# Optimization experiments

Measured on AMD Instinct MI355X. Metric: run time of the kernel, lower is better.

Reference implementation:

```python
import jax, jax.numpy as jnp
import numpy as np

B, S, D, H, F = 2, 2048, 1024, 16, 4096
DK = D // H
EPS = 1e-6


def _ln(x, g, b):
    mu = jnp.mean(x, axis=-1, keepdims=True)
    var = jnp.mean(jnp.square(x - mu), axis=-1, keepdims=True)
    return (x - mu) * jax.lax.rsqrt(var + EPS) * g + b


def setup_inputs() -> dict:
    key = jax.random.key(0)
    ks = jax.random.split(key, 8)
    sc = 0.02
    return {
        "x": jax.random.normal(ks[0], (B, S, D), jnp.float32),
        "wq": jax.random.normal(ks[1], (D, D), jnp.float32) * sc,
        "bq": jnp.zeros((D,), jnp.float32),
        "wk": jax.random.normal(ks[2], (D, D), jnp.float32) * sc,
        "bk": jnp.zeros((D,), jnp.float32),
        "wv": jax.random.normal(ks[3], (D, D), jnp.float32) * sc,
        "bv": jnp.zeros((D,), jnp.float32),
        "wo": jax.random.normal(ks[4], (D, D), jnp.float32) * sc,
        "bo": jnp.zeros((D,), jnp.float32),
        "w1": jax.random.normal(ks[5], (D, F), jnp.float32) * sc,
        "b1": jnp.zeros((F,), jnp.float32),
        "w2": jax.random.normal(ks[6], (F, D), jnp.float32) * sc,
        "b2": jnp.zeros((D,), jnp.float32),
        "g1": jnp.ones((D,), jnp.float32),
        "be1": jnp.zeros((D,), jnp.float32),
        "g2": jnp.ones((D,), jnp.float32),
        "be2": jnp.zeros((D,), jnp.float32),
    }


def reference(x, wq, bq, wk, bk, wv, bv, wo, bo, w1, b1, w2, b2, g1, be1, g2, be2):
    # Multi-head self-attention (no masks, eval-mode dropout = identity)
    q = (x @ wq + bq).reshape(B, S, H, DK)
    k = (x @ wk + bk).reshape(B, S, H, DK)
    v = (x @ wv + bv).reshape(B, S, H, DK)
    scale = 1.0 / (DK ** 0.5)
    score = jnp.einsum('bihd,bjhd->bhij', q, k) * scale  # [B,H,S,S]
    p = jax.nn.softmax(score, axis=-1)
    attn = jnp.einsum('bhij,bjhd->bihd', p, v).reshape(B, S, D)
    attn = attn @ wo + bo
    # residual + LayerNorm 1
    h = _ln(x + attn, g1, be1)
    # FFN (relu) + residual + LayerNorm 2
    ff = jax.nn.relu(h @ w1 + b1) @ w2 + b2
    return _ln(h + ff, g2, be2)
```

## Files before the change

### kernel.cpp

```cpp
#include <hip/hip_runtime.h>
#include <hip/hip_bf16.h>
#include <cmath>

typedef __bf16 bf16_t;
typedef __bf16 bf16x4 __attribute__((ext_vector_type(4)));
typedef __bf16 bf16x8 __attribute__((ext_vector_type(8)));
typedef float  f32x4  __attribute__((ext_vector_type(4)));

__device__ __forceinline__ void gld_lds16(const bf16_t* g, bf16_t* l) {
    __builtin_amdgcn_global_load_lds(
        (const __attribute__((address_space(1))) void*)g,
        (__attribute__((address_space(3))) void*)l,
        16, 0, 0);
}

__global__ __launch_bounds__(256) void cast_bf16_k(const float* __restrict__ in,
                                                   bf16_t* __restrict__ out, int n4) {
    int i = blockIdx.x * 256 + threadIdx.x;
    if (i >= n4) return;
    f32x4 v = ((const f32x4*)in)[i];
    bf16x4 o;
    o[0] = (bf16_t)v[0]; o[1] = (bf16_t)v[1]; o[2] = (bf16_t)v[2]; o[3] = (bf16_t)v[3];
    ((bf16x4*)out)[i] = o;
}

__global__ __launch_bounds__(256) void transpose_cast(const float* __restrict__ in,
                                                      bf16_t* __restrict__ out,
                                                      int K, int N) {
    __shared__ float tile[32][33];
    int n0 = blockIdx.x * 32, k0 = blockIdx.y * 32;
    int tx = threadIdx.x & 31;
    int ty = threadIdx.x >> 5;
#pragma unroll
    for (int i = 0; i < 4; i++) {
        int kk = ty + i * 8;
        tile[kk][tx] = in[(size_t)(k0 + kk) * N + n0 + tx];
    }
    __syncthreads();
#pragma unroll
    for (int i = 0; i < 4; i++) {
        int nn = ty + i * 8;
        out[(size_t)(n0 + nn) * K + k0 + tx] = (bf16_t)tile[tx][nn];
    }
}

template<int MT>
__global__ __launch_bounds__(256) void gemm_bt(const bf16_t* __restrict__ A,
                                               const bf16_t* __restrict__ Bt,
                                               const float* __restrict__ bias,
                                               float* __restrict__ Cf,
                                               bf16_t* __restrict__ Cb,
                                               int M, int N, int K, int relu,
                                               int nbm, int nbn) {
    constexpr int TM = MT * 32;
    __shared__ __attribute__((aligned(16))) bf16_t As[TM * 32];
    __shared__ __attribute__((aligned(16))) bf16_t Bs[128 * 32];
    const int tid  = threadIdx.x;
    const int lane = tid & 63;
    const int wave = tid >> 6;
    const int wm = wave & 1, wn = wave >> 1;

    const int span  = 8 * nbn;
    const int group = blockIdx.x / span;
    const int rem   = blockIdx.x % span;
    const int bm    = group * 8 + (rem & 7);
    const int bn    = rem >> 3;

    const int r4 = tid >> 2;
    const int kc = (tid & 3) * 8;
    const bf16_t* Ag = A  + (size_t)(bm * TM  + r4) * K + kc;
    const bf16_t* Bg = Bt + (size_t)(bn * 128 + r4) * K + kc;
    bf16_t* Asl = As + tid * 8;
    bf16_t* Bsl = Bs + tid * 8;

    f32x4 acc[MT][4] = {};
    const int mrow = lane & 15;
    const int q8   = (lane >> 4) * 8;

    for (int k0 = 0; k0 < K; k0 += 32) {
        __syncthreads();
#pragma unroll
        for (int i = 0; i < MT / 2; i++)
            gld_lds16(Ag + (size_t)(i * 64) * K + k0, Asl + i * 64 * 32);
        gld_lds16(Bg + k0,                  Bsl);
        gld_lds16(Bg + (size_t)64 * K + k0, Bsl + 64 * 32);
        __syncthreads();

        bf16x8 af[MT], bfr[4];
#pragma unroll
        for (int mt = 0; mt < MT; mt++)
            af[mt] = *(const bf16x8*)(As + (wm * (MT * 16) + mt * 16 + mrow) * 32 + q8);
#pragma unroll
        for (int nt = 0; nt < 4; nt++)
            bfr[nt] = *(const bf16x8*)(Bs + (wn * 64 + nt * 16 + mrow) * 32 + q8);
#pragma unroll
        for (int mt = 0; mt < MT; mt++)
#pragma unroll
            for (int nt = 0; nt < 4; nt++)
                acc[mt][nt] = __builtin_amdgcn_mfma_f32_16x16x32_bf16(
                    af[mt], bfr[nt], acc[mt][nt], 0, 0, 0);
    }

    const int rq = (lane >> 4) * 4;
#pragma unroll
    for (int mt = 0; mt < MT; mt++) {
        int row0 = bm * TM + wm * (MT * 16) + mt * 16 + rq;
#pragma unroll
        for (int nt = 0; nt < 4; nt++) {
            int col = bn * 128 + wn * 64 + nt * 16 + mrow;
            float bv = bias ? bias[col] : 0.f;
#pragma unroll
            for (int r = 0; r < 4; r++) {
                float v = acc[mt][nt][r] + bv;
                if (relu) v = fmaxf(v, 0.f);
                size_t idx = (size_t)(row0 + r) * N + col;
                if (Cf) Cf[idx] = v;
                if (Cb) Cb[idx] = (bf16_t)v;
            }
        }
    }
}

__global__ __launch_bounds__(256) void v_transpose(const bf16_t* __restrict__ QKVb,
                                                   bf16_t* __restrict__ Vt) {
    __shared__ __attribute__((aligned(16))) bf16_t Ts[64][72];
    const int t = threadIdx.x;
    const int s0 = blockIdx.x * 64, h = blockIdx.y, b = blockIdx.z;
    const bf16_t* src = QKVb + (size_t)(b * 2048 + s0) * 3072 + 2048 + h * 64;
#pragma unroll
    for (int p = 0; p < 2; p++) {
        int sl = (t >> 3) + p * 32, dc = (t & 7) * 8;
        *(bf16x8*)&Ts[sl][dc] = *(const bf16x8*)(src + (size_t)sl * 3072 + dc);
    }
    __syncthreads();
    bf16_t* dst = Vt + (size_t)(b * 16 + h) * 64 * 2048 + s0;
#pragma unroll
    for (int p = 0; p < 2; p++) {
        int dl = (t >> 3) + p * 32, sc = (t & 7) * 8;
        bf16x8 v;
#pragma unroll
        for (int j = 0; j < 8; j++) v[j] = Ts[sc + j][dl];
        *(bf16x8*)(dst + (size_t)dl * 2048 + sc) = v;
    }
}

__global__ __launch_bounds__(256) void flash_attn_mfma(
    const bf16_t* __restrict__ QKVb,
    const bf16_t* __restrict__ Vtg,
    bf16_t* __restrict__ Outb) {
    __shared__ __attribute__((aligned(16))) bf16_t Qs[2 * 64 * 32];
    __shared__ __attribute__((aligned(16))) bf16_t Ks[2 * 64 * 32];
    __shared__ __attribute__((aligned(16))) bf16_t Vs[2 * 64 * 32];
    __shared__ __attribute__((aligned(16))) bf16_t Ps[64 * 72];
    const int t = threadIdx.x;
    const int lane = t & 63, wave = t >> 6;
    const int g = lane >> 4, cl = lane & 15;
    const int b = blockIdx.z, h = blockIdx.y, q0 = blockIdx.x * 64;
    const int RS = 3072;
    const bf16_t* Qg = QKVb + (size_t)(b * 2048 + q0) * RS + h * 64;
    const bf16_t* Kg = QKVb + (size_t)(b * 2048) * RS + 1024 + h * 64;
    const bf16_t* Vg = Vtg + (size_t)(b * 16 + h) * 64 * 2048;

    const int sr = t >> 2;
    const int sc = (t & 3) * 8;

    gld_lds16(Qg + (size_t)sr * RS + sc,      Qs + t * 8);
    gld_lds16(Qg + (size_t)sr * RS + 32 + sc, Qs + 4096 + t * 8);

    f32x4 Oacc[4] = {};
    f32x4 Lacc = {};
    bf16x8 ones;
#pragma unroll
    for (int j = 0; j < 8; j++) ones[j] = (bf16_t)1.0f;

    const int qrow_s = (wave * 16 + cl) * 32 + g * 8;
    const int prow_w = (wave * 16 + cl) * 72;
    const float C = 0.125f * 1.4426950408889634f;

    for (int kt = 0; kt < 2048; kt += 64) {
        __syncthreads();
        gld_lds16(Kg + (size_t)(kt + sr) * RS + sc,       Ks + t * 8);
        gld_lds16(Kg + (size_t)(kt + sr) * RS + 32 + sc,  Ks + 4096 + t * 8);
        gld_lds16(Vg + (size_t)sr * 2048 + kt + sc,       Vs + t * 8);
        gld_lds16(Vg + (size_t)sr * 2048 + kt + 32 + sc,  Vs + 4096 + t * 8);
        __syncthreads();

        f32x4 Sacc[4] = {};
#pragma unroll
        for (int ks = 0; ks < 2; ks++) {
            bf16x8 bq = *(const bf16x8*)(Qs + ks * 4096 + qrow_s);
#pragma unroll
            for (int mt = 0; mt < 4; mt++) {
                bf16x8 ak = *(const bf16x8*)(Ks + ks * 4096 + (mt * 16 + cl) * 32 + g * 8);
                Sacc[mt] = __builtin_amdgcn_mfma_f32_16x16x32_bf16(ak, bq, Sacc[mt], 0, 0, 0);
            }
        }

#pragma unroll
        for (int mt = 0; mt < 4; mt++) {
            bf16x4 p4;
#pragma unroll
            for (int r = 0; r < 4; r++)
                p4[r] = (bf16_t)__builtin_amdgcn_exp2f(Sacc[mt][r] * C);
            *(bf16x4*)(Ps + prow_w + mt * 16 + g * 4) = p4;
        }

#pragma unroll
        for (int ks = 0; ks < 2; ks++) {
            bf16x8 ap = *(const bf16x8*)(Ps + prow_w + ks * 32 + g * 8);
            Lacc = __builtin_amdgcn_mfma_f32_16x16x32_bf16(ap, ones, Lacc, 0, 0, 0);
#pragma unroll
            for (int nt = 0; nt < 4; nt++) {
                bf16x8 bv = *(const bf16x8*)(Vs + ks * 4096 + (nt * 16 + cl) * 32 + g * 8);
                Oacc[nt] = __builtin_amdgcn_mfma_f32_16x16x32_bf16(ap, bv, Oacc[nt], 0, 0, 0);
            }
        }
    }

#pragma unroll
    for (int r = 0; r < 4; r++) {
        float inv = 1.f / Lacc[r];
        int qrow = q0 + wave * 16 + g * 4 + r;
        size_t base = (size_t)(b * 2048 + qrow) * 1024 + h * 64;
#pragma unroll
        for (int nt = 0; nt < 4; nt++)
            Outb[base + nt * 16 + cl] = (bf16_t)(Oacc[nt][r] * inv);
    }
}

__global__ __launch_bounds__(256) void resid_ln(const float* __restrict__ a,
                                                const float* __restrict__ b,
                                                const float* __restrict__ g,
                                                const float* __restrict__ be,
                                                float* __restrict__ outf,
                                                bf16_t* __restrict__ outb) {
    const int row = blockIdx.x, t = threadIdx.x;
    const size_t base = (size_t)row * 1024;
    f32x4 v = ((const f32x4*)(a + base))[t] + ((const f32x4*)(b + base))[t];
    float sum = v[0] + v[1] + v[2] + v[3];
    float sq  = v[0] * v[0] + v[1] * v[1] + v[2] * v[2] + v[3] * v[3];
#pragma unroll
    for (int o = 1; o < 64; o <<= 1) {
        sum += __shfl_xor(sum, o);
        sq  += __shfl_xor(sq, o);
    }
    __shared__ float red[8];
    int wave = t >> 6, lane = t & 63;
    if (lane == 0) { red[wave] = sum; red[4 + wave] = sq; }
    __syncthreads();
    sum = red[0] + red[1] + red[2] + red[3];
    sq  = red[4] + red[5] + red[6] + red[7];
    float mu  = sum * (1.f / 1024.f);
    float var = sq * (1.f / 1024.f) - mu * mu;
    float rs  = rsqrtf(var + 1e-6f);
    f32x4 g4 = ((const f32x4*)g)[t];
    f32x4 b4 = ((const f32x4*)be)[t];
    f32x4 o = (v - mu) * rs * g4 + b4;
    ((f32x4*)(outf + base))[t] = o;
    if (outb) {
        bf16x4 ob;
        ob[0] = (bf16_t)o[0]; ob[1] = (bf16_t)o[1]; ob[2] = (bf16_t)o[2]; ob[3] = (bf16_t)o[3];
        ((bf16x4*)(outb + base))[t] = ob;
    }
}

extern "C" void kernel_launch(void* const* d_in, const int* in_sizes, int n_in,
                              void* d_out, int out_size, void* d_ws, size_t ws_size,
                              hipStream_t stream) {
    (void)in_sizes; (void)n_in; (void)out_size; (void)ws_size;
    const float* x   = (const float*)d_in[0];
    const float* wq  = (const float*)d_in[1];
    const float* bq  = (const float*)d_in[2];
    const float* wk  = (const float*)d_in[3];
    const float* bk  = (const float*)d_in[4];
    const float* wv  = (const float*)d_in[5];
    const float* bv  = (const float*)d_in[6];
    const float* wo  = (const float*)d_in[7];
    const float* bo  = (const float*)d_in[8];
    const float* w1  = (const float*)d_in[9];
    const float* b1  = (const float*)d_in[10];
    const float* w2  = (const float*)d_in[11];
    const float* b2  = (const float*)d_in[12];
    const float* g1  = (const float*)d_in[13];
    const float* be1 = (const float*)d_in[14];
    const float* g2  = (const float*)d_in[15];
    const float* be2 = (const float*)d_in[16];
    float* out = (float*)d_out;

    char* ws = (char*)d_ws;
    const size_t MB = 1ull << 20;
    bf16_t* xb    = (bf16_t*)(ws + 0);
    bf16_t* WtQKV = (bf16_t*)(ws + 8 * MB);
    bf16_t* WtO   = (bf16_t*)(ws + 14 * MB);
    bf16_t* Wt1   = (bf16_t*)(ws + 16 * MB);
    bf16_t* Wt2   = (bf16_t*)(ws + 24 * MB);
    float*  bqkv  = (float*)(ws + 32 * MB);
    bf16_t* QKVb  = (bf16_t*)(ws + 33 * MB);
    bf16_t* Vt    = (bf16_t*)(ws + 57 * MB);
    bf16_t* ffb   = (bf16_t*)(ws + 33 * MB);
    float*  o     = (float*)(ws + 65 * MB);
    float*  f2    = (float*)(ws + 65 * MB);
    float*  hbuf  = (float*)(ws + 81 * MB);
    bf16_t* hb    = (bf16_t*)(ws + 97 * MB);
    bf16_t* ab    = xb;

    cast_bf16_k<<<4096, 256, 0, stream>>>(x, xb, 4096 * 1024 / 4);
    transpose_cast<<<dim3(32, 32),  256, 0, stream>>>(wq, WtQKV,               1024, 1024);
    transpose_cast<<<dim3(32, 32),  256, 0, stream>>>(wk, WtQKV + 1024 * 1024, 1024, 1024);
    transpose_cast<<<dim3(32, 32),  256, 0, stream>>>(wv, WtQKV + 2048 * 1024, 1024, 1024);
    transpose_cast<<<dim3(32, 32),  256, 0, stream>>>(wo, WtO, 1024, 1024);
    transpose_cast<<<dim3(128, 32), 256, 0, stream>>>(w1, Wt1, 1024, 4096);
    transpose_cast<<<dim3(32, 128), 256, 0, stream>>>(w2, Wt2, 4096, 1024);
    hipMemcpyAsync(bqkv,        bq, 1024 * 4, hipMemcpyDeviceToDevice, stream);
    hipMemcpyAsync(bqkv + 1024, bk, 1024 * 4, hipMemcpyDeviceToDevice, stream);
    hipMemcpyAsync(bqkv + 2048, bv, 1024 * 4, hipMemcpyDeviceToDevice, stream);
    gemm_bt<4><<<768, 256, 0, stream>>>(xb, WtQKV, bqkv, nullptr, QKVb,
                                        4096, 3072, 1024, 0, 32, 24);
    v_transpose<<<dim3(32, 16, 2), 256, 0, stream>>>(QKVb, Vt);
    flash_attn_mfma<<<dim3(32, 16, 2), 256, 0, stream>>>(QKVb, Vt, ab);
    gemm_bt<2><<<512, 256, 0, stream>>>(ab, WtO, bo, o, nullptr,
                                        4096, 1024, 1024, 0, 64, 8);
    resid_ln<<<4096, 256, 0, stream>>>(x, o, g1, be1, hbuf, hb);
    gemm_bt<4><<<1024, 256, 0, stream>>>(hb, Wt1, b1, nullptr, ffb,
                                         4096, 4096, 1024, 1, 32, 32);
    gemm_bt<2><<<512, 256, 0, stream>>>(ffb, Wt2, b2, f2, nullptr,
                                        4096, 1024, 4096, 0, 64, 8);
    resid_ln<<<4096, 256, 0, stream>>>(hbuf, f2, g2, be2, out, nullptr);
}
```

Measured before the change: 425.8 us.

## Fuse prep kernels, compute V transposed via GEMM, split-K output GEMMs

Merges the weight transpose-casts, the x cast and the bias copy into one prep launch, replacing seven kernels and three memcpys. V is now produced already transposed by a separate GEMM (Wv^T times x^T) instead of a QKV GEMM followed by a transpose kernel. The Wo and W2 GEMMs move to the larger tile with 2-way split-K, and the residual LayerNorm sums the two partial outputs. The GEMM main loop now stages 64 of K per barrier pair. The aim is fewer launches, more blocks for the narrow GEMMs and less barrier overhead, at the cost of extra fp32 partial-output traffic.

Result: faster. 410.6 us (-3.6%).

```diff
diff --git a/kernel.cpp b/kernel.cpp
--- a/kernel.cpp
+++ b/kernel.cpp
@@ -14,51 +14,68 @@
         16, 0, 0);
 }
 
-__global__ __launch_bounds__(256) void cast_bf16_k(const float* __restrict__ in,
-                                                   bf16_t* __restrict__ out, int n4) {
-    int i = blockIdx.x * 256 + threadIdx.x;
-    if (i >= n4) return;
-    f32x4 v = ((const f32x4*)in)[i];
-    bf16x4 o;
-    o[0] = (bf16_t)v[0]; o[1] = (bf16_t)v[1]; o[2] = (bf16_t)v[2]; o[3] = (bf16_t)v[3];
-    ((bf16x4*)out)[i] = o;
-}
-
-__global__ __launch_bounds__(256) void transpose_cast(const float* __restrict__ in,
-                                                      bf16_t* __restrict__ out,
-                                                      int K, int N) {
+struct PrepArgs {
+    const float* w[6]; bf16_t* wt[6];
+    int K[6], N[6], start[6];
+    const float* x; bf16_t* xb; int castStart;
+    const float* bq; const float* bk; float* bqkv; int biasStart;
+};
+
+__global__ __launch_bounds__(256) void prep(PrepArgs pa) {
     __shared__ float tile[32][33];
-    int n0 = blockIdx.x * 32, k0 = blockIdx.y * 32;
-    int tx = threadIdx.x & 31;
-    int ty = threadIdx.x >> 5;
-#pragma unroll
-    for (int i = 0; i < 4; i++) {
-        int kk = ty + i * 8;
-        tile[kk][tx] = in[(size_t)(k0 + kk) * N + n0 + tx];
-    }
-    __syncthreads();
-#pragma unroll
-    for (int i = 0; i < 4; i++) {
-        int nn = ty + i * 8;
-        out[(size_t)(n0 + nn) * K + k0 + tx] = (bf16_t)tile[tx][nn];
+    const int bid = blockIdx.x, t = threadIdx.x;
+    if (bid < pa.castStart) {
+        int mi = 0;
+#pragma unroll
+        for (int i = 1; i < 6; i++) if (bid >= pa.start[i]) mi = i;
+        const int tt  = bid - pa.start[mi];
+        const int nbx = pa.N[mi] >> 5;
+        const int n0 = (tt % nbx) * 32, k0 = (tt / nbx) * 32;
+        const float* in = pa.w[mi];
+        bf16_t* out = pa.wt[mi];
+        const int K = pa.K[mi], N = pa.N[mi];
+        const int tx = t & 31, ty = t >> 5;
+#pragma unroll
+        for (int i = 0; i < 4; i++) {
+            int kk = ty + i * 8;
+            tile[kk][tx] = in[(size_t)(k0 + kk) * N + n0 + tx];
+        }
+        __syncthreads();
+#pragma unroll
+        for (int i = 0; i < 4; i++) {
+            int nn = ty + i * 8;
+            out[(size_t)(n0 + nn) * K + k0 + tx] = (bf16_t)tile[tx][nn];
+        }
+    } else if (bid < pa.biasStart) {
+        int i = (bid - pa.castStart) * 256 + t;
+        f32x4 v = ((const f32x4*)pa.x)[i];
+        bf16x4 o;
+        o[0] = (bf16_t)v[0]; o[1] = (bf16_t)v[1]; o[2] = (bf16_t)v[2]; o[3] = (bf16_t)v[3];
+        ((bf16x4*)pa.xb)[i] = o;
+    } else {
+#pragma unroll
+        for (int j = 0; j < 8; j++) {
+            int idx = t * 8 + j;
+            pa.bqkv[idx] = idx < 1024 ? pa.bq[idx] : pa.bk[idx - 1024];
+        }
     }
 }
 
 template<int MT>
-__global__ __launch_bounds__(256) void gemm_bt(const bf16_t* __restrict__ A,
-                                               const bf16_t* __restrict__ Bt,
-                                               const float* __restrict__ bias,
-                                               float* __restrict__ Cf,
-                                               bf16_t* __restrict__ Cb,
-                                               int M, int N, int K, int relu,
-                                               int nbm, int nbn) {
+__global__ __launch_bounds__(256) void gemm_bt(
+    const bf16_t* __restrict__ A, const bf16_t* __restrict__ Bt,
+    const float* __restrict__ bias,
+    float* __restrict__ Cf, bf16_t* __restrict__ Cb,
+    int M, int N, int lda, int Kloc, int relu, int nbn, int bias_row,
+    long bt_bstride, long c_bstride) {
     constexpr int TM = MT * 32;
-    __shared__ __attribute__((aligned(16))) bf16_t As[TM * 32];
-    __shared__ __attribute__((aligned(16))) bf16_t Bs[128 * 32];
+    __shared__ __attribute__((aligned(16))) bf16_t As[2][TM * 32];
+    __shared__ __attribute__((aligned(16))) bf16_t Bs[2][128 * 32];
     const int tid  = threadIdx.x;
     const int lane = tid & 63;
     const int wave = tid >> 6;
     const int wm = wave & 1, wn = wave >> 1;
+    const int kh = blockIdx.z;
 
     const int span  = 8 * nbn;
     const int group = blockIdx.x / span;
@@ -66,39 +83,49 @@
     const int bm    = group * 8 + (rem & 7);
     const int bn    = rem >> 3;
 
+    const bf16_t* Bt_b = Bt + (size_t)blockIdx.y * bt_bstride;
+    float*  Cf_b = Cf ? Cf + (size_t)blockIdx.y * c_bstride + (size_t)kh * M * N : nullptr;
+    bf16_t* Cb_b = Cb ? Cb + (size_t)blockIdx.y * c_bstride : nullptr;
+    const int koff = kh * Kloc;
+
     const int r4 = tid >> 2;
     const int kc = (tid & 3) * 8;
-    const bf16_t* Ag = A  + (size_t)(bm * TM  + r4) * K + kc;
-    const bf16_t* Bg = Bt + (size_t)(bn * 128 + r4) * K + kc;
-    bf16_t* Asl = As + tid * 8;
-    bf16_t* Bsl = Bs + tid * 8;
+    const bf16_t* Ag = A    + (size_t)(bm * TM  + r4) * lda + koff + kc;
+    const bf16_t* Bg = Bt_b + (size_t)(bn * 128 + r4) * lda + koff + kc;
 
     f32x4 acc[MT][4] = {};
     const int mrow = lane & 15;
     const int q8   = (lane >> 4) * 8;
 
-    for (int k0 = 0; k0 < K; k0 += 32) {
-        __syncthreads();
-#pragma unroll
-        for (int i = 0; i < MT / 2; i++)
-            gld_lds16(Ag + (size_t)(i * 64) * K + k0, Asl + i * 64 * 32);
-        gld_lds16(Bg + k0,                  Bsl);
-        gld_lds16(Bg + (size_t)64 * K + k0, Bsl + 64 * 32);
-        __syncthreads();
-
-        bf16x8 af[MT], bfr[4];
-#pragma unroll
-        for (int mt = 0; mt < MT; mt++)
-            af[mt] = *(const bf16x8*)(As + (wm * (MT * 16) + mt * 16 + mrow) * 32 + q8);
-#pragma unroll
-        for (int nt = 0; nt < 4; nt++)
-            bfr[nt] = *(const bf16x8*)(Bs + (wn * 64 + nt * 16 + mrow) * 32 + q8);
-#pragma unroll
-        for (int mt = 0; mt < MT; mt++)
+    for (int k0 = 0; k0 < Kloc; k0 += 64) {
+        __syncthreads();
+#pragma unroll
+        for (int hh = 0; hh < 2; hh++) {
+#pragma unroll
+            for (int i = 0; i < MT / 2; i++)
+                gld_lds16(Ag + (size_t)(i * 64) * lda + k0 + hh * 32,
+                          &As[hh][i * 64 * 32] + tid * 8);
+            gld_lds16(Bg + k0 + hh * 32,                  &Bs[hh][0] + tid * 8);
+            gld_lds16(Bg + (size_t)64 * lda + k0 + hh * 32, &Bs[hh][64 * 32] + tid * 8);
+        }
+        __syncthreads();
+
+#pragma unroll
+        for (int hh = 0; hh < 2; hh++) {
+            bf16x8 af[MT], bfr[4];
+#pragma unroll
+            for (int mt = 0; mt < MT; mt++)
+                af[mt] = *(const bf16x8*)(&As[hh][(wm * (MT * 16) + mt * 16 + mrow) * 32 + q8]);
 #pragma unroll
             for (int nt = 0; nt < 4; nt++)
-                acc[mt][nt] = __builtin_amdgcn_mfma_f32_16x16x32_bf16(
-                    af[mt], bfr[nt], acc[mt][nt], 0, 0, 0);
+                bfr[nt] = *(const bf16x8*)(&Bs[hh][(wn * 64 + nt * 16 + mrow) * 32 + q8]);
+#pragma unroll
+            for (int mt = 0; mt < MT; mt++)
+#pragma unroll
+                for (int nt = 0; nt < 4; nt++)
+                    acc[mt][nt] = __builtin_amdgcn_mfma_f32_16x16x32_bf16(
+                        af[mt], bfr[nt], acc[mt][nt], 0, 0, 0);
+        }
     }
 
     const int rq = (lane >> 4) * 4;
@@ -108,44 +135,22 @@
 #pragma unroll
         for (int nt = 0; nt < 4; nt++) {
             int col = bn * 128 + wn * 64 + nt * 16 + mrow;
-            float bv = bias ? bias[col] : 0.f;
+            float bvc = (bias && kh == 0 && !bias_row) ? bias[col] : 0.f;
 #pragma unroll
             for (int r = 0; r < 4; r++) {
-                float v = acc[mt][nt][r] + bv;
+                float bb = (bias && kh == 0 && bias_row) ? bias[row0 + r] : bvc;
+                float v = acc[mt][nt][r] + bb;
                 if (relu) v = fmaxf(v, 0.f);
                 size_t idx = (size_t)(row0 + r) * N + col;
-                if (Cf) Cf[idx] = v;
-                if (Cb) Cb[idx] = (bf16_t)v;
+                if (Cf_b) Cf_b[idx] = v;
+                if (Cb_b) Cb_b[idx] = (bf16_t)v;
             }
         }
     }
 }
 
-__global__ __launch_bounds__(256) void v_transpose(const bf16_t* __restrict__ QKVb,
-                                                   bf16_t* __restrict__ Vt) {
-    __shared__ __attribute__((aligned(16))) bf16_t Ts[64][72];
-    const int t = threadIdx.x;
-    const int s0 = blockIdx.x * 64, h = blockIdx.y, b = blockIdx.z;
-    const bf16_t* src = QKVb + (size_t)(b * 2048 + s0) * 3072 + 2048 + h * 64;
-#pragma unroll
-    for (int p = 0; p < 2; p++) {
-        int sl = (t >> 3) + p * 32, dc = (t & 7) * 8;
-        *(bf16x8*)&Ts[sl][dc] = *(const bf16x8*)(src + (size_t)sl * 3072 + dc);
-    }
-    __syncthreads();
-    bf16_t* dst = Vt + (size_t)(b * 16 + h) * 64 * 2048 + s0;
-#pragma unroll
-    for (int p = 0; p < 2; p++) {
-        int dl = (t >> 3) + p * 32, sc = (t & 7) * 8;
-        bf16x8 v;
-#pragma unroll
-        for (int j = 0; j < 8; j++) v[j] = Ts[sc + j][dl];
-        *(bf16x8*)(dst + (size_t)dl * 2048 + sc) = v;
-    }
-}
-
 __global__ __launch_bounds__(256) void flash_attn_mfma(
-    const bf16_t* __restrict__ QKVb,
+    const bf16_t* __restrict__ QKb,
     const bf16_t* __restrict__ Vtg,
     bf16_t* __restrict__ Outb) {
     __shared__ __attribute__((aligned(16))) bf16_t Qs[2 * 64 * 32];
@@ -156,10 +161,10 @@
     const int lane = t & 63, wave = t >> 6;
     const int g = lane >> 4, cl = lane & 15;
     const int b = blockIdx.z, h = blockIdx.y, q0 = blockIdx.x * 64;
-    const int RS = 3072;
-    const bf16_t* Qg = QKVb + (size_t)(b * 2048 + q0) * RS + h * 64;
-    const bf16_t* Kg = QKVb + (size_t)(b * 2048) * RS + 1024 + h * 64;
-    const bf16_t* Vg = Vtg + (size_t)(b * 16 + h) * 64 * 2048;
+    const int RS = 2048;
+    const bf16_t* Qg = QKb + (size_t)(b * 2048 + q0) * RS + h * 64;
+    const bf16_t* Kg = QKb + (size_t)(b * 2048) * RS + 1024 + h * 64;
+    const bf16_t* Vg = Vtg + ((size_t)b * 1024 + h * 64) * 2048;
 
     const int sr = t >> 2;
     const int sc = (t & 3) * 8;
@@ -228,15 +233,17 @@
     }
 }
 
-__global__ __launch_bounds__(256) void resid_ln(const float* __restrict__ a,
-                                                const float* __restrict__ b,
-                                                const float* __restrict__ g,
-                                                const float* __restrict__ be,
-                                                float* __restrict__ outf,
-                                                bf16_t* __restrict__ outb) {
+__global__ __launch_bounds__(256) void resid_ln3(const float* __restrict__ a,
+                                                 const float* __restrict__ p0,
+                                                 const float* __restrict__ p1,
+                                                 const float* __restrict__ g,
+                                                 const float* __restrict__ be,
+                                                 float* __restrict__ outf,
+                                                 bf16_t* __restrict__ outb) {
     const int row = blockIdx.x, t = threadIdx.x;
     const size_t base = (size_t)row * 1024;
-    f32x4 v = ((const f32x4*)(a + base))[t] + ((const f32x4*)(b + base))[t];
+    f32x4 v = ((const f32x4*)(a + base))[t] + ((const f32x4*)(p0 + base))[t];
+    if (p1) v += ((const f32x4*)(p1 + base))[t];
     float sum = v[0] + v[1] + v[2] + v[3];
     float sq  = v[0] * v[0] + v[1] * v[1] + v[2] * v[2] + v[3] * v[3];
 #pragma unroll
@@ -295,35 +302,40 @@
     bf16_t* Wt1   = (bf16_t*)(ws + 16 * MB);
     bf16_t* Wt2   = (bf16_t*)(ws + 24 * MB);
     float*  bqkv  = (float*)(ws + 32 * MB);
-    bf16_t* QKVb  = (bf16_t*)(ws + 33 * MB);
-    bf16_t* Vt    = (bf16_t*)(ws + 57 * MB);
+    bf16_t* QKb   = (bf16_t*)(ws + 33 * MB);
+    bf16_t* Vt    = (bf16_t*)(ws + 49 * MB);
     bf16_t* ffb   = (bf16_t*)(ws + 33 * MB);
-    float*  o     = (float*)(ws + 65 * MB);
+    float*  oa    = (float*)(ws + 65 * MB);
     float*  f2    = (float*)(ws + 65 * MB);
-    float*  hbuf  = (float*)(ws + 81 * MB);
-    bf16_t* hb    = (bf16_t*)(ws + 97 * MB);
+    float*  hbuf  = (float*)(ws + 97 * MB);
+    bf16_t* hb    = (bf16_t*)(ws + 113 * MB);
     bf16_t* ab    = xb;
-
-    cast_bf16_k<<<4096, 256, 0, stream>>>(x, xb, 4096 * 1024 / 4);
-    transpose_cast<<<dim3(32, 32),  256, 0, stream>>>(wq, WtQKV,               1024, 1024);
-    transpose_cast<<<dim3(32, 32),  256, 0, stream>>>(wk, WtQKV + 1024 * 1024, 1024, 1024);
-    transpose_cast<<<dim3(32, 32),  256, 0, stream>>>(wv, WtQKV + 2048 * 1024, 1024, 1024);
-    transpose_cast<<<dim3(32, 32),  256, 0, stream>>>(wo, WtO, 1024, 1024);
-    transpose_cast<<<dim3(128, 32), 256, 0, stream>>>(w1, Wt1, 1024, 4096);
-    transpose_cast<<<dim3(32, 128), 256, 0, stream>>>(w2, Wt2, 4096, 1024);
-    hipMemcpyAsync(bqkv,        bq, 1024 * 4, hipMemcpyDeviceToDevice, stream);
-    hipMemcpyAsync(bqkv + 1024, bk, 1024 * 4, hipMemcpyDeviceToDevice, stream);
-    hipMemcpyAsync(bqkv + 2048, bv, 1024 * 4, hipMemcpyDeviceToDevice, stream);
-    gemm_bt<4><<<768, 256, 0, stream>>>(xb, WtQKV, bqkv, nullptr, QKVb,
-                                        4096, 3072, 1024, 0, 32, 24);
-    v_transpose<<<dim3(32, 16, 2), 256, 0, stream>>>(QKVb, Vt);
-    flash_attn_mfma<<<dim3(32, 16, 2), 256, 0, stream>>>(QKVb, Vt, ab);
-    gemm_bt<2><<<512, 256, 0, stream>>>(ab, WtO, bo, o, nullptr,
-                                        4096, 1024, 1024, 0, 64, 8);
-    resid_ln<<<4096, 256, 0, stream>>>(x, o, g1, be1, hbuf, hb);
+    const int MN = 4096 * 1024;
+
+    PrepArgs pa;
+    pa.w[0] = wq; pa.w[1] = wk; pa.w[2] = wv; pa.w[3] = wo; pa.w[4] = w1; pa.w[5] = w2;
+    pa.wt[0] = WtQKV; pa.wt[1] = WtQKV + 1024 * 1024; pa.wt[2] = WtQKV + 2048 * 1024;
+    pa.wt[3] = WtO; pa.wt[4] = Wt1; pa.wt[5] = Wt2;
+    int Ks[6] = {1024, 1024, 1024, 1024, 1024, 4096};
+    int Ns[6] = {1024, 1024, 1024, 1024, 4096, 1024};
+    int st[6] = {0, 1024, 2048, 3072, 4096, 8192};
+    for (int i = 0; i < 6; i++) { pa.K[i] = Ks[i]; pa.N[i] = Ns[i]; pa.start[i] = st[i]; }
+    pa.x = x; pa.xb = xb; pa.castStart = 12288;
+    pa.bq = bq; pa.bk = bk; pa.bqkv = bqkv; pa.biasStart = 12288 + 4096;
+    prep<<<12288 + 4096 + 1, 256, 0, stream>>>(pa);
+
+    gemm_bt<4><<<512, 256, 0, stream>>>(xb, WtQKV, bqkv, nullptr, QKb,
+                                        4096, 2048, 1024, 1024, 0, 16, 0, 0, 0);
+    gemm_bt<2><<<dim3(256, 2, 1), 256, 0, stream>>>(WtQKV + 2048 * 1024, xb, bv,
+                                        nullptr, Vt, 1024, 2048, 1024, 1024, 0, 16, 1,
+                                        (long)2048 * 1024, (long)1024 * 2048);
+    flash_attn_mfma<<<dim3(32, 16, 2), 256, 0, stream>>>(QKb, Vt, ab);
+    gemm_bt<4><<<dim3(256, 1, 2), 256, 0, stream>>>(ab, WtO, bo, oa, nullptr,
+                                        4096, 1024, 1024, 512, 0, 8, 0, 0, 0);
+    resid_ln3<<<4096, 256, 0, stream>>>(x, oa, oa + MN, g1, be1, hbuf, hb);
     gemm_bt<4><<<1024, 256, 0, stream>>>(hb, Wt1, b1, nullptr, ffb,
-                                         4096, 4096, 1024, 1, 32, 32);
-    gemm_bt<2><<<512, 256, 0, stream>>>(ffb, Wt2, b2, f2, nullptr,
-                                        4096, 1024, 4096, 0, 64, 8);
-    resid_ln<<<4096, 256, 0, stream>>>(hbuf, f2, g2, be2, out, nullptr);
-}
+                                         4096, 4096, 1024, 1024, 1, 32, 0, 0, 0);
+    gemm_bt<4><<<dim3(256, 1, 2), 256, 0, stream>>>(ffb, Wt2, b2, f2, nullptr,
+                                        4096, 1024, 4096, 2048, 0, 8, 0, 0, 0);
+    resid_ln3<<<4096, 256, 0, stream>>>(hbuf, f2, f2 + MN, g2, be2, out, nullptr);
+}
```
